# Kernel optimization log

Measured on AMD Instinct MI355X. Metric: run time of the kernel, lower is better.

Reference implementation:

```python
import jax, jax.numpy as jnp
import numpy as np

# Circuit structure constants (must match input_specs)
V, K, C = 128, 32, 256   # vars, input nodes per var, categories (V*K == N)
L, N, F = 4, 4096, 16    # layer pairs, sum nodes per layer, sum fan-in
E, B = 8192, 512         # product elements per layer, batch size
EPS = 1e-6


def setup_inputs() -> dict:
    key = jax.random.key(0)
    ks = jax.random.split(key, 6)
    return {
        "inputs": jax.random.randint(ks[0], (B, V), 0, C),
        "prod_child_ids": jax.random.randint(ks[1], (L, E, 2), 0, N),
        "sum_child_ids": jax.random.randint(ks[2], (L, N, F), 0, E),
        "input_params": jax.random.uniform(ks[3], (V, K, C), dtype=jnp.float32),
        "sum_params": jax.random.uniform(ks[4], (L, N, F), dtype=jnp.float32),
        "root_params": jax.random.uniform(ks[5], (N,), dtype=jnp.float32),
    }


def _forward(inputs, prod_child_ids, sum_child_ids, input_params, sum_params, root_params):
    # --- input layer: categorical leaves -> node_mars [V*K, B] (log space) ---
    lw_in = jnp.log(input_params + EPS)
    lw_in = lw_in - jax.nn.logsumexp(lw_in, axis=-1, keepdims=True)  # normalized log-params
    x = inputs.T  # [V, B]
    nm = lw_in[jnp.arange(V)[:, None, None], jnp.arange(K)[None, :, None], x[:, None, :]]  # [V, K, B]
    nm = nm.reshape(V * K, B)  # node_mars for leaves, V*K == N

    # --- normalized sum-layer log-weights ---
    lw_sum = jnp.log(sum_params + EPS)
    lw_sum = lw_sum - jax.nn.logsumexp(lw_sum, axis=-1, keepdims=True)  # [L, N, F]

    # --- alternating prod / sum layer groups (fixed small L) ---
    for l in range(L):
        # product layer: element_mars[e] = sum of child node_mars (log space add)
        em = nm[prod_child_ids[l, :, 0]] + nm[prod_child_ids[l, :, 1]]  # [E, B]
        # sum layer: node_mars[n] = logsumexp_j(element_mars[child j] + log w[n, j])
        ch = em[sum_child_ids[l]]  # [N, F, B] irregular gather
        nm = jax.nn.logsumexp(ch + lw_sum[l][:, :, None], axis=1)  # [N, B]

    # --- root sum node -> log-likelihoods [B] ---
    lr = jnp.log(root_params + EPS)
    lr = lr - jax.nn.logsumexp(lr)
    return jax.nn.logsumexp(nm + lr[:, None], axis=0)  # [B]


def reference(inputs, prod_child_ids, sum_child_ids, input_params, sum_params, root_params):
    return _forward(inputs, prod_child_ids, sum_child_ids, input_params, sum_params, root_params)
```

## Files before the change

kernel.cpp:

```cpp
#include <hip/hip_runtime.h>
#include <hip/hip_fp16.h>
#include <math.h>

#define V_ 128
#define K_ 32
#define C_ 256
#define L_ 4
#define N_ 4096
#define F_ 16
#define E_ 8192
#define B_ 512
#define EPS_ 1e-6f

__device__ __forceinline__ __half2 u2h(unsigned u) {
    __half2 h; *reinterpret_cast<unsigned*>(&h) = u; return h;
}
__device__ __forceinline__ unsigned h2u(__half2 h) {
    return *reinterpret_cast<unsigned*>(&h);
}
__device__ __forceinline__ __half b2h(unsigned short u) {
    __half h; *reinterpret_cast<unsigned short*>(&h) = u; return h;
}
__device__ __forceinline__ unsigned short h2b(__half h) {
    return *reinterpret_cast<unsigned short*>(&h);
}
__device__ __forceinline__ __half2 hmax2(__half2 a, __half2 b) {
    float2 fa = __half22float2(a), fb = __half22float2(b);
    return __floats2half2_rn(fmaxf(fa.x, fb.x), fmaxf(fa.y, fb.y));
}

__global__ __launch_bounds__(256) void prep_kernel(const float* __restrict__ sp,
                                                   const int* __restrict__ prod,
                                                   const int* __restrict__ sc,
                                                   const float* __restrict__ ip,
                                                   const float* __restrict__ rp,
                                                   unsigned* __restrict__ PIW,
                                                   unsigned* __restrict__ PP,
                                                   float* __restrict__ inv_row,
                                                   float* __restrict__ lrpsum) {
    int blk = blockIdx.x;
    int tid = threadIdx.x;
    if (blk < 64) {
        int idx = blk * 256 + tid;
        const float4* row4 = (const float4*)(sp + (size_t)idx * F_);
        float v[F_];
        float s = 0.f;
#pragma unroll
        for (int q = 0; q < 4; q++) {
            float4 r = row4[q];
            v[4*q+0] = r.x + EPS_; v[4*q+1] = r.y + EPS_;
            v[4*q+2] = r.z + EPS_; v[4*q+3] = r.w + EPS_;
            s += v[4*q+0] + v[4*q+1] + v[4*q+2] + v[4*q+3];
        }
        float inv = 1.f / s;
        const int* scr = sc + (size_t)idx * F_;
        unsigned* dst  = PIW + (size_t)idx * F_;
#pragma unroll
        for (int f = 0; f < F_; f++) {
            unsigned wbits = h2b(__float2half(v[f] * inv));
            dst[f] = (unsigned)(unsigned short)scr[f] | (wbits << 16);
        }
    } else if (blk < 192) {
        int idx = (blk - 64) * 256 + tid;
        int2 c  = ((const int2*)prod)[idx];
        PP[idx] = (unsigned)c.x | ((unsigned)c.y << 16);
    } else if (blk < 192 + 1024) {
        int rblk = blk - 192;
        int n    = rblk * 4 + (tid >> 6);
        int lane = tid & 63;
        const float* row = ip + (size_t)n * C_;
        float t = 0.f;
#pragma unroll
        for (int i = 0; i < 4; i++) t += row[lane + 64 * i] + EPS_;
#pragma unroll
        for (int off = 32; off; off >>= 1) t += __shfl_down(t, off, 64);
        if (lane == 0) inv_row[n] = 1.f / t;
    } else {
        __shared__ float smem[4];
        float acc = 0.f;
        for (int i = tid; i < N_; i += 256) acc += rp[i] + EPS_;
#pragma unroll
        for (int off = 32; off; off >>= 1) acc += __shfl_down(acc, off, 64);
        if ((tid & 63) == 0) smem[tid >> 6] = acc;
        __syncthreads();
        if (tid == 0) lrpsum[0] = __logf(smem[0] + smem[1] + smem[2] + smem[3]);
    }
}

__global__ __launch_bounds__(1024) void mega_kernel(const float* __restrict__ ip,
                                                    const int* __restrict__ inputs,
                                                    const float* __restrict__ inv_row,
                                                    const float* __restrict__ rp,
                                                    const unsigned* __restrict__ PIW,
                                                    const unsigned* __restrict__ PP,
                                                    const float* __restrict__ lrpsum,
                                                    float* __restrict__ out) {
    __shared__ unsigned nm[N_];
    __shared__ unsigned em[E_];
    __shared__ unsigned redm[16];
    __shared__ float    redf[32];
    int tid  = threadIdx.x;
    int lane = tid & 63;
    int w    = tid >> 6;
    int b0   = blockIdx.x * 2, b1 = b0 + 1;

    float2 u[4];
    float mx0 = 0.f, mx1 = 0.f;
#pragma unroll
    for (int p = 0; p < 4; p++) {
        int n  = p * 1024 + tid;
        int v  = n >> 5;
        int x0 = inputs[b0 * V_ + v];
        int x1 = inputs[b1 * V_ + v];
        float invr = inv_row[n];
        u[p].x = (ip[(size_t)n * C_ + x0] + EPS_) * invr;
        u[p].y = (ip[(size_t)n * C_ + x1] + EPS_) * invr;
        mx0 = fmaxf(mx0, u[p].x);
        mx1 = fmaxf(mx1, u[p].y);
    }
#pragma unroll
    for (int off = 32; off; off >>= 1) {
        mx0 = fmaxf(mx0, __shfl_down(mx0, off, 64));
        mx1 = fmaxf(mx1, __shfl_down(mx1, off, 64));
    }
    if (lane == 0) { redf[w] = mx0; redf[16 + w] = mx1; }
    __syncthreads();
    float m0 = redf[0], m1 = redf[16];
#pragma unroll
    for (int i = 1; i < 16; i++) { m0 = fmaxf(m0, redf[i]); m1 = fmaxf(m1, redf[16 + i]); }
    float inv0 = 1.f / m0, inv1 = 1.f / m1;
    float sg0 = __logf(m0), sg1 = __logf(m1);
#pragma unroll
    for (int p = 0; p < 4; p++)
        nm[p * 1024 + tid] = h2u(__floats2half2_rn(u[p].x * inv0, u[p].y * inv1));
    __syncthreads();

    __half2 ha  = __floats2half2_rn(1.f, 1.f);
    float   af0 = 1.f, af1 = 1.f;

    for (int l = 0; l < L_ - 1; l++) {
        const uint4* pp4 = (const uint4*)(PP + (size_t)l * E_);
#pragma unroll
        for (int p = 0; p < 2; p++) {
            uint4 c = pp4[p * 1024 + tid];
            int e   = (p * 1024 + tid) * 4;
            em[e+0] = h2u(__hmul2(__hmul2(u2h(nm[c.x & 0xffff]), ha),
                                  __hmul2(u2h(nm[c.x >> 16]), ha)));
            em[e+1] = h2u(__hmul2(__hmul2(u2h(nm[c.y & 0xffff]), ha),
                                  __hmul2(u2h(nm[c.y >> 16]), ha)));
            em[e+2] = h2u(__hmul2(__hmul2(u2h(nm[c.z & 0xffff]), ha),
                                  __hmul2(u2h(nm[c.z >> 16]), ha)));
            em[e+3] = h2u(__hmul2(__hmul2(u2h(nm[c.w & 0xffff]), ha),
                                  __hmul2(u2h(nm[c.w >> 16]), ha)));
        }
        sg0 = 2.f * sg0 + 2.f * __logf(af0);
        sg1 = 2.f * sg1 + 2.f * __logf(af1);
        sg0 -= 4.f * __logf(af0) * 0.f;
        __syncthreads();

        const unsigned* piw = PIW + (size_t)l * N_ * F_;
        __half2 hm = u2h(0u);
#pragma unroll
        for (int p = 0; p < 4; p++) {
            int n = p * 1024 + tid;
            const uint4* qv = (const uint4*)(piw + (size_t)n * F_);
            uint4 q0 = qv[0], q1 = qv[1], q2 = qv[2], q3 = qv[3];
            __half2 acc = u2h(0u);
            unsigned qq;
            qq = q0.x; acc = __hfma2(u2h(em[qq & 0xffff]), __half2half2(b2h((unsigned short)(qq >> 16))), acc);
            qq = q0.y; acc = __hfma2(u2h(em[qq & 0xffff]), __half2half2(b2h((unsigned short)(qq >> 16))), acc);
            qq = q0.z; acc = __hfma2(u2h(em[qq & 0xffff]), __half2half2(b2h((unsigned short)(qq >> 16))), acc);
            qq = q0.w; acc = __hfma2(u2h(em[qq & 0xffff]), __half2half2(b2h((unsigned short)(qq >> 16))), acc);
            qq = q1.x; acc = __hfma2(u2h(em[qq & 0xffff]), __half2half2(b2h((unsigned short)(qq >> 16))), acc);
            qq = q1.y; acc = __hfma2(u2h(em[qq & 0xffff]), __half2half2(b2h((unsigned short)(qq >> 16))), acc);
            qq = q1.z; acc = __hfma2(u2h(em[qq & 0xffff]), __half2half2(b2h((unsigned short)(qq >> 16))), acc);
            qq = q1.w; acc = __hfma2(u2h(em[qq & 0xffff]), __half2half2(b2h((unsigned short)(qq >> 16))), acc);
            qq = q2.x; acc = __hfma2(u2h(em[qq & 0xffff]), __half2half2(b2h((unsigned short)(qq >> 16))), acc);
            qq = q2.y; acc = __hfma2(u2h(em[qq & 0xffff]), __half2half2(b2h((unsigned short)(qq >> 16))), acc);
            qq = q2.z; acc = __hfma2(u2h(em[qq & 0xffff]), __half2half2(b2h((unsigned short)(qq >> 16))), acc);
            qq = q2.w; acc = __hfma2(u2h(em[qq & 0xffff]), __half2half2(b2h((unsigned short)(qq >> 16))), acc);
            qq = q3.x; acc = __hfma2(u2h(em[qq & 0xffff]), __half2half2(b2h((unsigned short)(qq >> 16))), acc);
            qq = q3.y; acc = __hfma2(u2h(em[qq & 0xffff]), __half2half2(b2h((unsigned short)(qq >> 16))), acc);
            qq = q3.z; acc = __hfma2(u2h(em[qq & 0xffff]), __half2half2(b2h((unsigned short)(qq >> 16))), acc);
            qq = q3.w; acc = __hfma2(u2h(em[qq & 0xffff]), __half2half2(b2h((unsigned short)(qq >> 16))), acc);
            nm[n] = h2u(acc);
            hm    = hmax2(hm, acc);
        }
#pragma unroll
        for (int off = 32; off; off >>= 1)
            hm = hmax2(hm, u2h(__shfl_down(h2u(hm), off, 64)));
        if (lane == 0) redm[w] = h2u(hm);
        __syncthreads();
        __half2 M = u2h(redm[0]);
#pragma unroll
        for (int i = 1; i < 16; i++) M = hmax2(M, u2h(redm[i]));
        float M0 = __half2float(__low2half(M)), M1 = __half2float(__high2half(M));
        ha  = __floats2half2_rn(fminf(1.f / M0, 60000.f), fminf(1.f / M1, 60000.f));
        af0 = __half2float(__low2half(ha));
        af1 = __half2float(__high2half(ha));
        sg0 -= 2.f * __logf(af0);
        sg1 -= 2.f * __logf(af1);
    }

    {
        const uint4* pp4 = (const uint4*)(PP + (size_t)(L_ - 1) * E_);
#pragma unroll
        for (int p = 0; p < 2; p++) {
            uint4 c = pp4[p * 1024 + tid];
            int e   = (p * 1024 + tid) * 4;
            em[e+0] = h2u(__hmul2(__hmul2(u2h(nm[c.x & 0xffff]), ha),
                                  __hmul2(u2h(nm[c.x >> 16]), ha)));
            em[e+1] = h2u(__hmul2(__hmul2(u2h(nm[c.y & 0xffff]), ha),
                                  __hmul2(u2h(nm[c.y >> 16]), ha)));
            em[e+2] = h2u(__hmul2(__hmul2(u2h(nm[c.z & 0xffff]), ha),
                                  __hmul2(u2h(nm[c.z >> 16]), ha)));
            em[e+3] = h2u(__hmul2(__hmul2(u2h(nm[c.w & 0xffff]), ha),
                                  __hmul2(u2h(nm[c.w >> 16]), ha)));
        }
        sg0 = 2.f * sg0 + 2.f * __logf(af0);
        sg1 = 2.f * sg1 + 2.f * __logf(af1);
        __syncthreads();

        const unsigned* piw = PIW + (size_t)(L_ - 1) * N_ * F_;
        float S0 = 0.f, S1 = 0.f;
#pragma unroll
        for (int p = 0; p < 4; p++) {
            int n = p * 1024 + tid;
            const uint4* qv = (const uint4*)(piw + (size_t)n * F_);
            uint4 qa = qv[0], qb = qv[1], qc = qv[2], qd = qv[3];
            __half2 acc = u2h(0u);
            unsigned qq;
            qq = qa.x; acc = __hfma2(u2h(em[qq & 0xffff]), __half2half2(b2h((unsigned short)(qq >> 16))), acc);
            qq = qa.y; acc = __hfma2(u2h(em[qq & 0xffff]), __half2half2(b2h((unsigned short)(qq >> 16))), acc);
            qq = qa.z; acc = __hfma2(u2h(em[qq & 0xffff]), __half2half2(b2h((unsigned short)(qq >> 16))), acc);
            qq = qa.w; acc = __hfma2(u2h(em[qq & 0xffff]), __half2half2(b2h((unsigned short)(qq >> 16))), acc);
            qq = qb.x; acc = __hfma2(u2h(em[qq & 0xffff]), __half2half2(b2h((unsigned short)(qq >> 16))), acc);
            qq = qb.y; acc = __hfma2(u2h(em[qq & 0xffff]), __half2half2(b2h((unsigned short)(qq >> 16))), acc);
            qq = qb.z; acc = __hfma2(u2h(em[qq & 0xffff]), __half2half2(b2h((unsigned short)(qq >> 16))), acc);
            qq = qb.w; acc = __hfma2(u2h(em[qq & 0xffff]), __half2half2(b2h((unsigned short)(qq >> 16))), acc);
            qq = qc.x; acc = __hfma2(u2h(em[qq & 0xffff]), __half2half2(b2h((unsigned short)(qq >> 16))), acc);
            qq = qc.y; acc = __hfma2(u2h(em[qq & 0xffff]), __half2half2(b2h((unsigned short)(qq >> 16))), acc);
            qq = qc.z; acc = __hfma2(u2h(em[qq & 0xffff]), __half2half2(b2h((unsigned short)(qq >> 16))), acc);
            qq = qc.w; acc = __hfma2(u2h(em[qq & 0xffff]), __half2half2(b2h((unsigned short)(qq >> 16))), acc);
            qq = qd.x; acc = __hfma2(u2h(em[qq & 0xffff]), __half2half2(b2h((unsigned short)(qq >> 16))), acc);
            qq = qd.y; acc = __hfma2(u2h(em[qq & 0xffff]), __half2half2(b2h((unsigned short)(qq >> 16))), acc);
            qq = qd.z; acc = __hfma2(u2h(em[qq & 0xffff]), __half2half2(b2h((unsigned short)(qq >> 16))), acc);
            qq = qd.w; acc = __hfma2(u2h(em[qq & 0xffff]), __half2half2(b2h((unsigned short)(qq >> 16))), acc);
            float2 vv = __half22float2(acc);
            float  r  = rp[n] + EPS_;
            S0 += r * vv.x;
            S1 += r * vv.y;
        }
#pragma unroll
        for (int off = 32; off; off >>= 1) {
            S0 += __shfl_down(S0, off, 64);
            S1 += __shfl_down(S1, off, 64);
        }
        if (lane == 0) { redf[w] = S0; redf[16 + w] = S1; }
        __syncthreads();
        if (tid == 0) {
            float s0 = 0.f, s1 = 0.f;
#pragma unroll
            for (int i = 0; i < 16; i++) { s0 += redf[i]; s1 += redf[16 + i]; }
            float lr = lrpsum[0];
            out[b0] = __logf(s0) + sg0 - lr;
            out[b1] = __logf(s1) + sg1 - lr;
        }
    }
}

extern "C" void kernel_launch(void* const* d_in, const int* in_sizes, int n_in,
                              void* d_out, int out_size, void* d_ws, size_t ws_size,
                              hipStream_t stream) {
    const int*   inputs = (const int*)d_in[0];
    const int*   prod   = (const int*)d_in[1];
    const int*   sc     = (const int*)d_in[2];
    const float* ip     = (const float*)d_in[3];
    const float* sp     = (const float*)d_in[4];
    const float* rp     = (const float*)d_in[5];
    float* out = (float*)d_out;

    unsigned* PIW     = (unsigned*)d_ws;
    unsigned* PP      = PIW + (size_t)L_ * N_ * F_;
    float*    inv_row = (float*)(PP + (size_t)L_ * E_);
    float*    lrpsum  = inv_row + N_;

    prep_kernel<<<64 + 128 + 1024 + 1, 256, 0, stream>>>(sp, prod, sc, ip, rp,
                                                         PIW, PP, inv_row, lrpsum);
    mega_kernel<<<B_ / 2, 1024, 0, stream>>>(ip, inputs, inv_row, rp,
                                             PIW, PP, lrpsum, out);
}
```

Baseline: 108.9 us.

## Pre-scale packed indices to byte offsets, interleave PIW layout, split FMA chains

The prep kernel now stores sum-child and product-child indices pre-shifted to byte offsets. It also writes PIW in a plane-major layout (4 planes of N uint4), so each thread's global loads across a wave are coalesced instead of strided by 64 bytes. The mega kernel uses byte-offset LDS addressing, a perm builtin to broadcast the fp16 weight, vectorized uint4 stores of product results, and two independent accumulators to shorten the hfma dependency chain. Reassociating the sum into two fp16 partials slightly changes rounding.

```diff
diff --git a/kernel.cpp b/kernel.cpp
--- a/kernel.cpp
+++ b/kernel.cpp
@@ -42,6 +42,8 @@
     int tid = threadIdx.x;
     if (blk < 64) {
         int idx = blk * 256 + tid;
+        int l   = idx >> 12;
+        int n   = idx & (N_ - 1);
         const float4* row4 = (const float4*)(sp + (size_t)idx * F_);
         float v[F_];
         float s = 0.f;
@@ -54,16 +56,24 @@
         }
         float inv = 1.f / s;
         const int* scr = sc + (size_t)idx * F_;
-        unsigned* dst  = PIW + (size_t)idx * F_;
-#pragma unroll
-        for (int f = 0; f < F_; f++) {
-            unsigned wbits = h2b(__float2half(v[f] * inv));
-            dst[f] = (unsigned)(unsigned short)scr[f] | (wbits << 16);
+        uint4* dst = (uint4*)PIW + ((size_t)l * 4) * N_ + n;
+#pragma unroll
+        for (int q = 0; q < 4; q++) {
+            uint4 o;
+            o.x = (unsigned)(unsigned short)(scr[4*q+0] << 2) |
+                  ((unsigned)h2b(__float2half(v[4*q+0] * inv)) << 16);
+            o.y = (unsigned)(unsigned short)(scr[4*q+1] << 2) |
+                  ((unsigned)h2b(__float2half(v[4*q+1] * inv)) << 16);
+            o.z = (unsigned)(unsigned short)(scr[4*q+2] << 2) |
+                  ((unsigned)h2b(__float2half(v[4*q+2] * inv)) << 16);
+            o.w = (unsigned)(unsigned short)(scr[4*q+3] << 2) |
+                  ((unsigned)h2b(__float2half(v[4*q+3] * inv)) << 16);
+            dst[(size_t)q * N_] = o;
         }
     } else if (blk < 192) {
         int idx = (blk - 64) * 256 + tid;
         int2 c  = ((const int2*)prod)[idx];
-        PP[idx] = (unsigned)c.x | ((unsigned)c.y << 16);
+        PP[idx] = ((unsigned)c.x << 2) | ((unsigned)c.y << 18);
     } else if (blk < 192 + 1024) {
         int rblk = blk - 192;
         int n    = rblk * 4 + (tid >> 6);
@@ -86,6 +96,16 @@
         if (tid == 0) lrpsum[0] = __logf(smem[0] + smem[1] + smem[2] + smem[3]);
     }
 }
+
+
+#define SSTEP(QQ, ACC) { unsigned q_ = (QQ); \
+    (ACC) = __hfma2(u2h(*(const unsigned*)((const char*)em + (q_ & 0xfffcu))), \
+                    u2h(__builtin_amdgcn_perm(q_, q_, 0x03020302u)), (ACC)); }
+
+#define PSTEP(QQ, DST) { unsigned q_ = (QQ); \
+    __half2 t0_ = __hmul2(u2h(*(const unsigned*)((const char*)nm + (q_ & 0xfffcu))), ha); \
+    __half2 t1_ = __hmul2(u2h(*(const unsigned*)((const char*)nm + (q_ >> 16))), ha); \
+    (DST) = h2u(__hmul2(t0_, t1_)); }
 
 __global__ __launch_bounds__(1024) void mega_kernel(const float* __restrict__ ip,
                                                     const int* __restrict__ inputs,
@@ -95,8 +115,8 @@
                                                     const unsigned* __restrict__ PP,
                                                     const float* __restrict__ lrpsum,
                                                     float* __restrict__ out) {
-    __shared__ unsigned nm[N_];
-    __shared__ unsigned em[E_];
+    __shared__ __align__(16) unsigned em[E_];
+    __shared__ __align__(16) unsigned nm[N_];
     __shared__ unsigned redm[16];
     __shared__ float    redf[32];
     int tid  = threadIdx.x;
@@ -143,46 +163,29 @@
 #pragma unroll
         for (int p = 0; p < 2; p++) {
             uint4 c = pp4[p * 1024 + tid];
-            int e   = (p * 1024 + tid) * 4;
-            em[e+0] = h2u(__hmul2(__hmul2(u2h(nm[c.x & 0xffff]), ha),
-                                  __hmul2(u2h(nm[c.x >> 16]), ha)));
-            em[e+1] = h2u(__hmul2(__hmul2(u2h(nm[c.y & 0xffff]), ha),
-                                  __hmul2(u2h(nm[c.y >> 16]), ha)));
-            em[e+2] = h2u(__hmul2(__hmul2(u2h(nm[c.z & 0xffff]), ha),
-                                  __hmul2(u2h(nm[c.z >> 16]), ha)));
-            em[e+3] = h2u(__hmul2(__hmul2(u2h(nm[c.w & 0xffff]), ha),
-                                  __hmul2(u2h(nm[c.w >> 16]), ha)));
+            uint4 o;
+            PSTEP(c.x, o.x); PSTEP(c.y, o.y); PSTEP(c.z, o.z); PSTEP(c.w, o.w);
+            ((uint4*)em)[p * 1024 + tid] = o;
         }
         sg0 = 2.f * sg0 + 2.f * __logf(af0);
         sg1 = 2.f * sg1 + 2.f * __logf(af1);
-        sg0 -= 4.f * __logf(af0) * 0.f;
-        __syncthreads();
-
-        const unsigned* piw = PIW + (size_t)l * N_ * F_;
+        __syncthreads();
+
+        const uint4* piw4 = (const uint4*)PIW + (size_t)l * 4 * N_;
         __half2 hm = u2h(0u);
 #pragma unroll
         for (int p = 0; p < 4; p++) {
             int n = p * 1024 + tid;
-            const uint4* qv = (const uint4*)(piw + (size_t)n * F_);
-            uint4 q0 = qv[0], q1 = qv[1], q2 = qv[2], q3 = qv[3];
-            __half2 acc = u2h(0u);
-            unsigned qq;
-            qq = q0.x; acc = __hfma2(u2h(em[qq & 0xffff]), __half2half2(b2h((unsigned short)(qq >> 16))), acc);
-            qq = q0.y; acc = __hfma2(u2h(em[qq & 0xffff]), __half2half2(b2h((unsigned short)(qq >> 16))), acc);
-            qq = q0.z; acc = __hfma2(u2h(em[qq & 0xffff]), __half2half2(b2h((unsigned short)(qq >> 16))), acc);
-            qq = q0.w; acc = __hfma2(u2h(em[qq & 0xffff]), __half2half2(b2h((unsigned short)(qq >> 16))), acc);
-            qq = q1.x; acc = __hfma2(u2h(em[qq & 0xffff]), __half2half2(b2h((unsigned short)(qq >> 16))), acc);
-            qq = q1.y; acc = __hfma2(u2h(em[qq & 0xffff]), __half2half2(b2h((unsigned short)(qq >> 16))), acc);
-            qq = q1.z; acc = __hfma2(u2h(em[qq & 0xffff]), __half2half2(b2h((unsigned short)(qq >> 16))), acc);
-            qq = q1.w; acc = __hfma2(u2h(em[qq & 0xffff]), __half2half2(b2h((unsigned short)(qq >> 16))), acc);
-            qq = q2.x; acc = __hfma2(u2h(em[qq & 0xffff]), __half2half2(b2h((unsigned short)(qq >> 16))), acc);
-            qq = q2.y; acc = __hfma2(u2h(em[qq & 0xffff]), __half2half2(b2h((unsigned short)(qq >> 16))), acc);
-            qq = q2.z; acc = __hfma2(u2h(em[qq & 0xffff]), __half2half2(b2h((unsigned short)(qq >> 16))), acc);
-            qq = q2.w; acc = __hfma2(u2h(em[qq & 0xffff]), __half2half2(b2h((unsigned short)(qq >> 16))), acc);
-            qq = q3.x; acc = __hfma2(u2h(em[qq & 0xffff]), __half2half2(b2h((unsigned short)(qq >> 16))), acc);
-            qq = q3.y; acc = __hfma2(u2h(em[qq & 0xffff]), __half2half2(b2h((unsigned short)(qq >> 16))), acc);
-            qq = q3.z; acc = __hfma2(u2h(em[qq & 0xffff]), __half2half2(b2h((unsigned short)(qq >> 16))), acc);
-            qq = q3.w; acc = __hfma2(u2h(em[qq & 0xffff]), __half2half2(b2h((unsigned short)(qq >> 16))), acc);
+            uint4 q0 = piw4[n];
+            uint4 q1 = piw4[N_ + n];
+            uint4 q2 = piw4[2 * N_ + n];
+            uint4 q3 = piw4[3 * N_ + n];
+            __half2 a0 = u2h(0u), a1 = u2h(0u);
+            SSTEP(q0.x, a0) SSTEP(q0.y, a1) SSTEP(q0.z, a0) SSTEP(q0.w, a1)
+            SSTEP(q1.x, a0) SSTEP(q1.y, a1) SSTEP(q1.z, a0) SSTEP(q1.w, a1)
+            SSTEP(q2.x, a0) SSTEP(q2.y, a1) SSTEP(q2.z, a0) SSTEP(q2.w, a1)
+            SSTEP(q3.x, a0) SSTEP(q3.y, a1) SSTEP(q3.z, a0) SSTEP(q3.w, a1)
+            __half2 acc = __hadd2(a0, a1);
             nm[n] = h2u(acc);
             hm    = hmax2(hm, acc);
         }
@@ -207,46 +210,29 @@
 #pragma unroll
         for (int p = 0; p < 2; p++) {
             uint4 c = pp4[p * 1024 + tid];
-            int e   = (p * 1024 + tid) * 4;
-            em[e+0] = h2u(__hmul2(__hmul2(u2h(nm[c.x & 0xffff]), ha),
-                                  __hmul2(u2h(nm[c.x >> 16]), ha)));
-            em[e+1] = h2u(__hmul2(__hmul2(u2h(nm[c.y & 0xffff]), ha),
-                                  __hmul2(u2h(nm[c.y >> 16]), ha)));
-            em[e+2] = h2u(__hmul2(__hmul2(u2h(nm[c.z & 0xffff]), ha),
-                                  __hmul2(u2h(nm[c.z >> 16]), ha)));
-            em[e+3] = h2u(__hmul2(__hmul2(u2h(nm[c.w & 0xffff]), ha),
-                                  __hmul2(u2h(nm[c.w >> 16]), ha)));
+            uint4 o;
+            PSTEP(c.x, o.x); PSTEP(c.y, o.y); PSTEP(c.z, o.z); PSTEP(c.w, o.w);
+            ((uint4*)em)[p * 1024 + tid] = o;
         }
         sg0 = 2.f * sg0 + 2.f * __logf(af0);
         sg1 = 2.f * sg1 + 2.f * __logf(af1);
         __syncthreads();
 
-        const unsigned* piw = PIW + (size_t)(L_ - 1) * N_ * F_;
+        const uint4* piw4 = (const uint4*)PIW + (size_t)(L_ - 1) * 4 * N_;
         float S0 = 0.f, S1 = 0.f;
 #pragma unroll
         for (int p = 0; p < 4; p++) {
             int n = p * 1024 + tid;
-            const uint4* qv = (const uint4*)(piw + (size_t)n * F_);
-            uint4 qa = qv[0], qb = qv[1], qc = qv[2], qd = qv[3];
-            __half2 acc = u2h(0u);
-            unsigned qq;
-            qq = qa.x; acc = __hfma2(u2h(em[qq & 0xffff]), __half2half2(b2h((unsigned short)(qq >> 16))), acc);
-            qq = qa.y; acc = __hfma2(u2h(em[qq & 0xffff]), __half2half2(b2h((unsigned short)(qq >> 16))), acc);
-            qq = qa.z; acc = __hfma2(u2h(em[qq & 0xffff]), __half2half2(b2h((unsigned short)(qq >> 16))), acc);
-            qq = qa.w; acc = __hfma2(u2h(em[qq & 0xffff]), __half2half2(b2h((unsigned short)(qq >> 16))), acc);
-            qq = qb.x; acc = __hfma2(u2h(em[qq & 0xffff]), __half2half2(b2h((unsigned short)(qq >> 16))), acc);
-            qq = qb.y; acc = __hfma2(u2h(em[qq & 0xffff]), __half2half2(b2h((unsigned short)(qq >> 16))), acc);
-            qq = qb.z; acc = __hfma2(u2h(em[qq & 0xffff]), __half2half2(b2h((unsigned short)(qq >> 16))), acc);
-            qq = qb.w; acc = __hfma2(u2h(em[qq & 0xffff]), __half2half2(b2h((unsigned short)(qq >> 16))), acc);
-            qq = qc.x; acc = __hfma2(u2h(em[qq & 0xffff]), __half2half2(b2h((unsigned short)(qq >> 16))), acc);
-            qq = qc.y; acc = __hfma2(u2h(em[qq & 0xffff]), __half2half2(b2h((unsigned short)(qq >> 16))), acc);
-            qq = qc.z; acc = __hfma2(u2h(em[qq & 0xffff]), __half2half2(b2h((unsigned short)(qq >> 16))), acc);
-            qq = qc.w; acc = __hfma2(u2h(em[qq & 0xffff]), __half2half2(b2h((unsigned short)(qq >> 16))), acc);
-            qq = qd.x; acc = __hfma2(u2h(em[qq & 0xffff]), __half2half2(b2h((unsigned short)(qq >> 16))), acc);
-            qq = qd.y; acc = __hfma2(u2h(em[qq & 0xffff]), __half2half2(b2h((unsigned short)(qq >> 16))), acc);
-            qq = qd.z; acc = __hfma2(u2h(em[qq & 0xffff]), __half2half2(b2h((unsigned short)(qq >> 16))), acc);
-            qq = qd.w; acc = __hfma2(u2h(em[qq & 0xffff]), __half2half2(b2h((unsigned short)(qq >> 16))), acc);
-            float2 vv = __half22float2(acc);
+            uint4 q0 = piw4[n];
+            uint4 q1 = piw4[N_ + n];
+            uint4 q2 = piw4[2 * N_ + n];
+            uint4 q3 = piw4[3 * N_ + n];
+            __half2 a0 = u2h(0u), a1 = u2h(0u);
+            SSTEP(q0.x, a0) SSTEP(q0.y, a1) SSTEP(q0.z, a0) SSTEP(q0.w, a1)
+            SSTEP(q1.x, a0) SSTEP(q1.y, a1) SSTEP(q1.z, a0) SSTEP(q1.w, a1)
+            SSTEP(q2.x, a0) SSTEP(q2.y, a1) SSTEP(q2.z, a0) SSTEP(q2.w, a1)
+            SSTEP(q3.x, a0) SSTEP(q3.y, a1) SSTEP(q3.z, a0) SSTEP(q3.w, a1)
+            float2 vv = __half22float2(__hadd2(a0, a1));
             float  r  = rp[n] + EPS_;
             S0 += r * vv.x;
             S1 += r * vv.y;
```

After: 105.5 us. -3.1%, faster.
